# Kernel tuning notes

Measured on AMD Instinct MI355X. Metric: run time of the kernel, lower is better.

## Reference

```python
import jax, jax.numpy as jnp
import numpy as np


def setup_inputs() -> dict:
    key = jax.random.key(0)
    ks = jax.random.split(key, 12)
    B, IN, H = 4096, 512, 1024
    s = lambda k, shape, scale: jax.random.normal(k, shape, dtype=jnp.float32) * scale
    inp = {
        "inputs": s(ks[0], (B, IN), 1.0),
        "h0": s(ks[1], (B, H), 1.0),
        "c0": s(ks[2], (B, H), 1.0),
        "ts": jax.random.uniform(ks[3], (B, 2), dtype=jnp.float32),
        "w_ih": s(ks[4], (4 * H, IN), 1.0 / np.sqrt(IN)),
        "w_hh": s(ks[5], (4 * H, H), 1.0 / np.sqrt(H)),
        "b_ih": s(ks[6], (4 * H,), 1.0 / np.sqrt(H)),
        "b_hh": s(ks[7], (4 * H,), 1.0 / np.sqrt(H)),
        "w1": s(ks[8], (H, H), 1.0 / np.sqrt(H)),
        "b1": s(ks[9], (H,), 1.0 / np.sqrt(H)),
        "w2": s(ks[10], (H, H), 1.0 / np.sqrt(H)),
        "b2": s(ks[11], (H,), 1.0 / np.sqrt(H)),
    }
    return inp


def _lstm_cell(x, h, c, w_ih, w_hh, b_ih, b_hh):
    # gates: [B, 4H] in PyTorch (i, f, g, o) order
    gates = x @ w_ih.T + h @ w_hh.T + b_ih + b_hh
    i, f, g, o = jnp.split(gates, 4, axis=-1)
    i, f, o = jax.nn.sigmoid(i), jax.nn.sigmoid(f), jax.nn.sigmoid(o)
    g = jnp.tanh(g)
    c_new = f * c + i * g
    h_new = o * jnp.tanh(c_new)
    return h_new, c_new


def reference(inputs, h0, c0, ts, w_ih, w_hh, b_ih, b_hh, w1, b1, w2, b2):
    # Two stacked LSTMCell applications sharing the same weights
    h, c = _lstm_cell(inputs, h0, c0, w_ih, w_hh, b_ih, b_hh)
    h, c = _lstm_cell(inputs, h, c, w_ih, w_hh, b_ih, b_hh)

    # Autonomous ODE func: Linear -> Tanh -> Linear
    f = lambda y: jnp.tanh(y @ w1.T + b1) @ w2.T + b2

    # One RK4 step per sample from ts[:,0] to ts[:,1] (batched, no python loop)
    dt = (ts[:, 1] - ts[:, 0])[:, None]  # [B, 1]
    k1 = f(h)
    k2 = f(h + 0.5 * dt * k1)
    k3 = f(h + 0.5 * dt * k2)
    k4 = f(h + dt * k3)
    ht = h + (dt / 6.0) * (k1 + 2.0 * k2 + 2.0 * k3 + k4)
    return (ht, c)
```

## Files before the change

kernel.cpp:

```cpp
#include <hip/hip_runtime.h>

typedef short short8 __attribute__((ext_vector_type(8)));
typedef float f32x4 __attribute__((ext_vector_type(4)));
typedef unsigned short u16x8 __attribute__((ext_vector_type(8)));

#define B_DIM 4096
#define IN_DIM 512
#define H_DIM 1024
#define KCAT 1536

__device__ __forceinline__ float bs2f(unsigned short s) {
    return __uint_as_float(((unsigned int)s) << 16);
}
__device__ __forceinline__ unsigned short f2bs(float f) {
    unsigned int u = __float_as_uint(f);
    u += 0x7fff + ((u >> 16) & 1);
    return (unsigned short)(u >> 16);
}
__device__ __forceinline__ float sigm(float x) { return 1.0f / (1.0f + __expf(-x)); }
__device__ __forceinline__ float ftanh(float x) { return 1.0f - 2.0f / (__expf(2.0f * x) + 1.0f); }

__device__ __forceinline__ int gperm(int r) {
    int g = r >> 10, j = r & 1023;
    return ((j >> 4) << 6) + (g << 4) + (j & 15);
}

#define T0 262144
#define T1 786432
#define T2 1048576
#define T3 1572864
#define T4 1703936
#define T5 1835008
__device__ __forceinline__ u16x8 cvt8(const float* __restrict__ in, long i) {
    float4 a = *(const float4*)(in + i);
    float4 b = *(const float4*)(in + i + 4);
    u16x8 o;
    o[0] = f2bs(a.x); o[1] = f2bs(a.y); o[2] = f2bs(a.z); o[3] = f2bs(a.w);
    o[4] = f2bs(b.x); o[5] = f2bs(b.y); o[6] = f2bs(b.z); o[7] = f2bs(b.w);
    return o;
}
__global__ __launch_bounds__(256) void pack_all(const float* __restrict__ x,
                                                const float* __restrict__ h0,
                                                const float* __restrict__ wih,
                                                const float* __restrict__ whh,
                                                const float* __restrict__ w1,
                                                const float* __restrict__ w2,
                                                unsigned short* __restrict__ xb,
                                                unsigned short* __restrict__ hb0,
                                                unsigned short* __restrict__ wcat,
                                                unsigned short* __restrict__ w116,
                                                unsigned short* __restrict__ w216) {
    long g = (long)blockIdx.x * 256 + threadIdx.x;
    if (g < T0) {
        long i = g * 8;
        *(u16x8*)(xb + i) = cvt8(x, i);
    } else if (g < T1) {
        long i = (g - T0) * 8;
        *(u16x8*)(hb0 + i) = cvt8(h0, i);
    } else if (g < T2) {
        long i = (g - T1) * 8;
        int r = (int)(i / IN_DIM), c = (int)(i % IN_DIM);
        *(u16x8*)(wcat + (size_t)gperm(r) * KCAT + c) = cvt8(wih, i);
    } else if (g < T3) {
        long i = (g - T2) * 8;
        int r = (int)(i / H_DIM), c = (int)(i % H_DIM);
        *(u16x8*)(wcat + (size_t)gperm(r) * KCAT + IN_DIM + c) = cvt8(whh, i);
    } else if (g < T4) {
        long i = (g - T3) * 8;
        *(u16x8*)(w116 + i) = cvt8(w1, i);
    } else if (g < T5) {
        long i = (g - T4) * 8;
        *(u16x8*)(w216 + i) = cvt8(w2, i);
    }
}

__global__ __launch_bounds__(256) void prep_small(const float* __restrict__ bih,
                                                  const float* __restrict__ bhh,
                                                  const float* __restrict__ ts,
                                                  float* __restrict__ bsum,
                                                  float* __restrict__ dtv,
                                                  int n4h, int nb) {
    int i = blockIdx.x * blockDim.x + threadIdx.x;
    if (i < n4h) bsum[gperm(i)] = bih[i] + bhh[i];
    if (i < nb)  dtv[i] = ts[2 * i + 1] - ts[2 * i];
}

#define NT8 (KCAT / 32)

__global__ __launch_bounds__(512) void gemm8(
    const unsigned short* __restrict__ xb,
    const unsigned short* __restrict__ hb,
    const unsigned short* __restrict__ W,
    const float* __restrict__ bias,
    unsigned short* __restrict__ h_out,
    float* __restrict__ c_out,
    const float* __restrict__ c_in) {
    __shared__ unsigned short lA[3][128 * 32];
    __shared__ unsigned short lB[3][256 * 32];
    const int t = threadIdx.x;
    const int lane = t & 63;
    const int wave = t >> 6;
    const int wm = (wave >> 2) * 64;
    const int wn = (wave & 3) * 64;
    const int fr = lane & 15;
    const int kb = lane >> 4;
    const int tile_m = blockIdx.y * 128;
    const int tile_n = blockIdx.x * 256;

    f32x4 acc[4][4];
    #pragma unroll
    for (int i = 0; i < 4; ++i)
        #pragma unroll
        for (int j = 0; j < 4; ++j)
            acc[i][j] = (f32x4){0.f, 0.f, 0.f, 0.f};

    auto stageA = [&](int kt) {
        const int buf = kt % 3;
        int row = t >> 2;
        int g = t & 3;
        int gs = g ^ ((row >> 1) & 3);
        int kk = kt * 32 + gs * 8;
        const unsigned short* src = (kk < IN_DIM)
            ? xb + (size_t)(tile_m + row) * IN_DIM + kk
            : hb + (size_t)(tile_m + row) * H_DIM + (kk - IN_DIM);
        __builtin_amdgcn_global_load_lds(
            (__attribute__((address_space(1))) void*)src,
            (__attribute__((address_space(3))) void*)(&lA[buf][row * 32 + g * 8]), 16, 0, 0);
    };
    auto stageB = [&](int kt) {
        const int buf = kt % 3;
        #pragma unroll
        for (int j = 0; j < 2; ++j) {
            int idx = j * 512 + t;
            int row = idx >> 2;
            int g = idx & 3;
            int gs = g ^ ((row >> 1) & 3);
            int kk = kt * 32 + gs * 8;
            __builtin_amdgcn_global_load_lds(
                (__attribute__((address_space(1))) void*)(W + (size_t)(tile_n + row) * KCAT + kk),
                (__attribute__((address_space(3))) void*)(&lB[buf][row * 32 + g * 8]), 16, 0, 0);
        }
    };

    stageA(0); stageB(0);
    stageA(1); stageB(1);

    for (int kt = 0; kt < NT8; ++kt) {
        const int buf = kt % 3;
        if (kt + 1 < NT8) asm volatile("s_waitcnt vmcnt(3)" ::: "memory");
        else              asm volatile("s_waitcnt vmcnt(0)" ::: "memory");
        __builtin_amdgcn_s_barrier();
        asm volatile("" ::: "memory");
        short8 bfr[4], af[4];
        #pragma unroll
        for (int j = 0; j < 4; ++j) {
            int brow = wn + j * 16 + fr;
            bfr[j] = *(const short8*)&lB[buf][brow * 32 + (kb ^ ((brow >> 1) & 3)) * 8];
        }
        #pragma unroll
        for (int i = 0; i < 4; ++i) {
            int arow = wm + i * 16 + fr;
            af[i] = *(const short8*)&lA[buf][arow * 32 + (kb ^ ((arow >> 1) & 3)) * 8];
        }
        __builtin_amdgcn_s_setprio(1);
        #pragma unroll
        for (int i = 0; i < 4; ++i)
            #pragma unroll
            for (int j = 0; j < 4; ++j)
                acc[i][j] = __builtin_amdgcn_mfma_f32_16x16x32_bf16(af[i], bfr[j], acc[i][j], 0, 0, 0);
        __builtin_amdgcn_s_setprio(0);
        if (kt + 2 < NT8) { stageA(kt + 2); stageB(kt + 2); }
        asm volatile("" ::: "memory");
    }

    const int jbase = ((tile_n + wn) >> 6) << 4;
    float bv[4];
    #pragma unroll
    for (int g = 0; g < 4; ++g) bv[g] = bias[tile_n + wn + g * 16 + fr];
    #pragma unroll
    for (int i = 0; i < 4; ++i) {
        #pragma unroll
        for (int r = 0; r < 4; ++r) {
            const int m = tile_m + wm + i * 16 + kb * 4 + r;
            const int j = jbase + fr;
            float ig = sigm(acc[i][0][r] + bv[0]);
            float fg = sigm(acc[i][1][r] + bv[1]);
            float gg = ftanh(acc[i][2][r] + bv[2]);
            float og = sigm(acc[i][3][r] + bv[3]);
            float cin = c_in[(size_t)m * H_DIM + j];
            float cn = fg * cin + ig * gg;
            float hn = og * ftanh(cn);
            h_out[(size_t)m * H_DIM + j] = f2bs(hn);
            c_out[(size_t)m * H_DIM + j] = cn;
        }
    }
}

template <int EPI>
__global__ __launch_bounds__(256) void gemm2(
    const unsigned short* __restrict__ A1,
    const unsigned short* __restrict__ W,
    const int M, const int N, const int K,
    const float* __restrict__ bias,
    unsigned short* __restrict__ outb,
    float* __restrict__ outf,
    const unsigned short* __restrict__ hmat,
    const float* __restrict__ dtv,
    float* __restrict__ S,
    unsigned short* __restrict__ ynext,
    const float alpha, const float cw, const int first) {
    constexpr int BM = 64, BN = 64, BK = 64;
    constexpr int MR = 2, NR = 2;
    __shared__ unsigned short lA[2][BM * BK];
    __shared__ unsigned short lB[2][BN * BK];
    const int t = threadIdx.x;
    const int lane = t & 63;
    const int wave = t >> 6;
    const int wm = (wave >> 1) * 32;
    const int wn = (wave & 1) * 32;
    const int fr = lane & 15;
    const int kb = lane >> 4;
    const int tile_m = blockIdx.y * BM;
    const int tile_n = blockIdx.x * BN;

    f32x4 acc[MR][NR];
    #pragma unroll
    for (int i = 0; i < MR; ++i)
        #pragma unroll
        for (int j = 0; j < NR; ++j)
            acc[i][j] = (f32x4){0.f, 0.f, 0.f, 0.f};

    const unsigned short* aptr1 = A1 + (size_t)tile_m * K;
    const unsigned short* wptr  = W + (size_t)tile_n * K;

    auto stage = [&](int kt) {
        const int buf = kt & 1;
        const int k0 = kt * BK;
        #pragma unroll
        for (int j = 0; j < 2; ++j) {
            int idx = j * 256 + t;
            int row = idx >> 3;
            int g = idx & 7;
            int col = (g ^ (row & 7)) * 8;
            __builtin_amdgcn_global_load_lds(
                (__attribute__((address_space(1))) void*)(aptr1 + (size_t)row * K + k0 + col),
                (__attribute__((address_space(3))) void*)(&lA[buf][row * BK + g * 8]), 16, 0, 0);
        }
        #pragma unroll
        for (int j = 0; j < 2; ++j) {
            int idx = j * 256 + t;
            int row = idx >> 3;
            int g = idx & 7;
            int col = (g ^ (row & 7)) * 8;
            __builtin_amdgcn_global_load_lds(
                (__attribute__((address_space(1))) void*)(wptr + (size_t)row * K + k0 + col),
                (__attribute__((address_space(3))) void*)(&lB[buf][row * BK + g * 8]), 16, 0, 0);
        }
    };

    const int NT = K / BK;
    stage(0);
    for (int kt = 0; kt < NT; ++kt) {
        const int buf = kt & 1;
        asm volatile("s_waitcnt vmcnt(0)" ::: "memory");
        __builtin_amdgcn_s_barrier();
        asm volatile("" ::: "memory");
        short8 af[2][MR], bfr[2][NR];
        #pragma unroll
        for (int h = 0; h < 2; ++h) {
            #pragma unroll
            for (int i = 0; i < MR; ++i) {
                int arow = wm + i * 16 + fr;
                int gidx = h * 4 + kb;
                af[h][i] = *(const short8*)&lA[buf][arow * BK + (gidx ^ (arow & 7)) * 8];
            }
            #pragma unroll
            for (int j = 0; j < NR; ++j) {
                int brow = wn + j * 16 + fr;
                int gidx = h * 4 + kb;
                bfr[h][j] = *(const short8*)&lB[buf][brow * BK + (gidx ^ (brow & 7)) * 8];
            }
        }
        if (kt + 1 < NT) stage(kt + 1);
        #pragma unroll
        for (int h = 0; h < 2; ++h)
            #pragma unroll
            for (int i = 0; i < MR; ++i)
                #pragma unroll
                for (int j = 0; j < NR; ++j)
                    acc[i][j] = __builtin_amdgcn_mfma_f32_16x16x32_bf16(af[h][i], bfr[h][j], acc[i][j], 0, 0, 0);
        asm volatile("" ::: "memory");
    }

    #pragma unroll
    for (int i = 0; i < MR; ++i) {
        #pragma unroll
        for (int r = 0; r < 4; ++r) {
            const int m = tile_m + wm + i * 16 + kb * 4 + r;
            float dt = 0.f;
            if (EPI >= 2) dt = dtv[m];
            #pragma unroll
            for (int j = 0; j < NR; ++j) {
                const int n = tile_n + wn + j * 16 + fr;
                const size_t off = (size_t)m * N + n;
                float v = acc[i][j][r];
                if (bias) v += bias[n];
                if (EPI == 1) {
                    outb[off] = f2bs(ftanh(v));
                } else if (EPI == 2) {
                    float hv = bs2f(hmat[off]);
                    float s = first ? 0.f : S[off];
                    S[off] = s + cw * v;
                    ynext[off] = f2bs(hv + alpha * dt * v);
                } else {
                    float hv = bs2f(hmat[off]);
                    outf[off] = hv + (dt * (1.0f / 6.0f)) * (S[off] + v);
                }
            }
        }
    }
}

extern "C" void kernel_launch(void* const* d_in, const int* in_sizes, int n_in,
                              void* d_out, int out_size, void* d_ws, size_t ws_size,
                              hipStream_t stream) {
    int IX = 0, IH0 = 1, IC0 = 2, ITS = 3, IWIH = 4, IWHH = 5, IBIH = 6, IBHH = 7,
        IW1 = 8, IB1 = 9, IW2 = 10, IB2 = 11;
    const bool sorted_ok = n_in >= 12 &&
        in_sizes[0] == 1024 && in_sizes[1] == 1024 && in_sizes[2] == 4096 &&
        in_sizes[3] == 4096 && in_sizes[4] == 4194304 && in_sizes[5] == 4194304 &&
        in_sizes[6] == 2097152 && in_sizes[7] == 8192 && in_sizes[8] == 1048576 &&
        in_sizes[9] == 1048576 && in_sizes[10] == 4194304 && in_sizes[11] == 2097152;
    if (sorted_ok) {
        IB1 = 0; IB2 = 1; IBHH = 2; IBIH = 3; IC0 = 4; IH0 = 5;
        IX = 6; ITS = 7; IW1 = 8; IW2 = 9; IWHH = 10; IWIH = 11;
    }
    const float* x_f   = (const float*)d_in[IX];
    const float* h0_f  = (const float*)d_in[IH0];
    const float* c0_f  = (const float*)d_in[IC0];
    const float* ts_f  = (const float*)d_in[ITS];
    const float* wih_f = (const float*)d_in[IWIH];
    const float* whh_f = (const float*)d_in[IWHH];
    const float* bih_f = (const float*)d_in[IBIH];
    const float* bhh_f = (const float*)d_in[IBHH];
    const float* w1_f  = (const float*)d_in[IW1];
    const float* b1_f  = (const float*)d_in[IB1];
    const float* w2_f  = (const float*)d_in[IW2];
    const float* b2_f  = (const float*)d_in[IB2];

    constexpr size_t SZ_BIN  = (size_t)B_DIM * IN_DIM;
    constexpr size_t SZ_BH   = (size_t)B_DIM * H_DIM;
    constexpr size_t SZ_HH   = (size_t)H_DIM * H_DIM;
    constexpr size_t SZ_WCAT = (size_t)4 * H_DIM * KCAT;

    float* bsum = (float*)d_ws;
    float* dtv  = bsum + 4 * H_DIM;
    float* S    = dtv + B_DIM;
    float* c1f  = S + SZ_BH;
    unsigned short* wcat = (unsigned short*)(c1f + SZ_BH);
    unsigned short* w116 = wcat + SZ_WCAT;
    unsigned short* w216 = w116 + SZ_HH;
    unsigned short* xb   = w216 + SZ_HH;
    unsigned short* hb0  = xb + SZ_BIN;
    unsigned short* hb1  = hb0 + SZ_BH;
    unsigned short* hb2  = hb1 + SZ_BH;
    unsigned short* ubuf = hb2 + SZ_BH;
    unsigned short* ybuf = ubuf + SZ_BH;

    float* out_ht = (float*)d_out;
    float* out_c  = out_ht + SZ_BH;

    const int TB = 256;
    pack_all<<<T5 / TB, TB, 0, stream>>>(x_f, h0_f, wih_f, whh_f, w1_f, w2_f,
                                         xb, hb0, wcat, w116, w216);
    prep_small<<<(4 * H_DIM) / TB, TB, 0, stream>>>(bih_f, bhh_f, ts_f, bsum, dtv, 4 * H_DIM, B_DIM);

    dim3 g8(4 * H_DIM / 256, B_DIM / 128);
    dim3 gSm(H_DIM / 64, B_DIM / 64);

    gemm8<<<g8, 512, 0, stream>>>(xb, hb0, wcat, bsum, hb1, c1f, c0_f);
    gemm8<<<g8, 512, 0, stream>>>(xb, hb1, wcat, bsum, hb2, out_c, c1f);

    gemm2<1><<<gSm, TB, 0, stream>>>(
        hb2, w116, B_DIM, H_DIM, H_DIM, b1_f,
        ubuf, nullptr, nullptr, nullptr, nullptr, nullptr, 0.f, 0.f, 0);
    gemm2<2><<<gSm, TB, 0, stream>>>(
        ubuf, w216, B_DIM, H_DIM, H_DIM, b2_f,
        nullptr, nullptr, hb2, dtv, S, ybuf, 0.5f, 1.0f, 1);
    gemm2<1><<<gSm, TB, 0, stream>>>(
        ybuf, w116, B_DIM, H_DIM, H_DIM, b1_f,
        ubuf, nullptr, nullptr, nullptr, nullptr, nullptr, 0.f, 0.f, 0);
    gemm2<2><<<gSm, TB, 0, stream>>>(
        ubuf, w216, B_DIM, H_DIM, H_DIM, b2_f,
        nullptr, nullptr, hb2, dtv, S, ybuf, 0.5f, 2.0f, 0);
    gemm2<1><<<gSm, TB, 0, stream>>>(
        ybuf, w116, B_DIM, H_DIM, H_DIM, b1_f,
        ubuf, nullptr, nullptr, nullptr, nullptr, nullptr, 0.f, 0.f, 0);
    gemm2<2><<<gSm, TB, 0, stream>>>(
        ubuf, w216, B_DIM, H_DIM, H_DIM, b2_f,
        nullptr, nullptr, hb2, dtv, S, ybuf, 1.0f, 2.0f, 0);
    gemm2<1><<<gSm, TB, 0, stream>>>(
        ybuf, w116, B_DIM, H_DIM, H_DIM, b1_f,
        ubuf, nullptr, nullptr, nullptr, nullptr, nullptr, 0.f, 0.f, 0);
    gemm2<3><<<gSm, TB, 0, stream>>>(
        ubuf, w216, B_DIM, H_DIM, H_DIM, b2_f,
        nullptr, out_ht, hb2, dtv, S, nullptr, 0.f, 0.f, 0);
}
```

Measured before the change: 328.9 us.

## Fold W2 into W1 to cut RK4 GEMM chain from eight to five

```diff
diff --git a/kernel.cpp b/kernel.cpp
--- a/kernel.cpp
+++ b/kernel.cpp
@@ -74,6 +74,35 @@
     }
 }
 
+__global__ __launch_bounds__(256) void transp_w2(const float* __restrict__ w2,
+                                                 unsigned short* __restrict__ w2t) {
+    int tid = blockIdx.x * 256 + threadIdx.x;
+    int t = tid & 1023;
+    int jb = tid >> 10;
+    float4 a = *(const float4*)(w2 + (size_t)t * H_DIM + jb * 8);
+    float4 b = *(const float4*)(w2 + (size_t)t * H_DIM + jb * 8 + 4);
+    float v[8] = {a.x, a.y, a.z, a.w, b.x, b.y, b.z, b.w};
+    #pragma unroll
+    for (int q = 0; q < 8; ++q)
+        w2t[(size_t)(jb * 8 + q) * H_DIM + t] = f2bs(v[q]);
+}
+
+__global__ __launch_bounds__(256) void bck(const float* __restrict__ b2,
+                                           const float* __restrict__ w1,
+                                           float* __restrict__ bc) {
+    __shared__ float ws[4];
+    int n = blockIdx.x;
+    int t = threadIdx.x;
+    float4 bv = *(const float4*)(b2 + t * 4);
+    float4 wv = *(const float4*)(w1 + (size_t)n * H_DIM + t * 4);
+    float p = bv.x * wv.x + bv.y * wv.y + bv.z * wv.z + bv.w * wv.w;
+    #pragma unroll
+    for (int off = 32; off > 0; off >>= 1) p += __shfl_down(p, off);
+    if ((t & 63) == 0) ws[t >> 6] = p;
+    __syncthreads();
+    if (t == 0) bc[n] = ws[0] + ws[1] + ws[2] + ws[3];
+}
+
 __global__ __launch_bounds__(256) void prep_small(const float* __restrict__ bih,
                                                   const float* __restrict__ bhh,
                                                   const float* __restrict__ ts,
@@ -204,11 +233,11 @@
     const float* __restrict__ bias,
     unsigned short* __restrict__ outb,
     float* __restrict__ outf,
+    const float* __restrict__ z1f,
+    float* __restrict__ Uf,
     const unsigned short* __restrict__ hmat,
     const float* __restrict__ dtv,
-    float* __restrict__ S,
-    unsigned short* __restrict__ ynext,
-    const float alpha, const float cw, const int first) {
+    const float alpha, const float cw, const int first, const int last) {
     constexpr int BM = 64, BN = 64, BK = 64;
     constexpr int MR = 2, NR = 2;
     __shared__ unsigned short lA[2][BM * BK];
@@ -298,23 +327,36 @@
         for (int r = 0; r < 4; ++r) {
             const int m = tile_m + wm + i * 16 + kb * 4 + r;
             float dt = 0.f;
-            if (EPI >= 2) dt = dtv[m];
+            if (EPI >= 6) dt = dtv[m];
             #pragma unroll
             for (int j = 0; j < NR; ++j) {
                 const int n = tile_n + wn + j * 16 + fr;
                 const size_t off = (size_t)m * N + n;
                 float v = acc[i][j][r];
-                if (bias) v += bias[n];
-                if (EPI == 1) {
+                if (EPI == 0) {
+                    if (bias) v += bias[n];
+                    outb[off] = f2bs(v);
+                } else if (EPI == 5) {
+                    v += bias[n];
+                    outf[off] = v;
                     outb[off] = f2bs(ftanh(v));
-                } else if (EPI == 2) {
-                    float hv = bs2f(hmat[off]);
-                    float s = first ? 0.f : S[off];
-                    S[off] = s + cw * v;
-                    ynext[off] = f2bs(hv + alpha * dt * v);
+                } else if (EPI == 6) {
+                    v += bias[n];
+                    float z1v = z1f[off];
+                    float z = z1v + alpha * dt * v;
+                    float u = ftanh(z);
+                    if (first) {
+                        Uf[off] = ftanh(z1v) + cw * u;
+                        outb[off] = f2bs(u);
+                    } else if (last) {
+                        outb[off] = f2bs(Uf[off] + cw * u);
+                    } else {
+                        Uf[off] = Uf[off] + cw * u;
+                        outb[off] = f2bs(u);
+                    }
                 } else {
                     float hv = bs2f(hmat[off]);
-                    outf[off] = hv + (dt * (1.0f / 6.0f)) * (S[off] + v);
+                    outf[off] = hv + dt * (v * (1.0f / 6.0f) + bias[n]);
                 }
             }
         }
@@ -355,12 +397,15 @@
 
     float* bsum = (float*)d_ws;
     float* dtv  = bsum + 4 * H_DIM;
-    float* S    = dtv + B_DIM;
+    float* bc   = dtv + B_DIM;
+    float* S    = bc + H_DIM;
     float* c1f  = S + SZ_BH;
     unsigned short* wcat = (unsigned short*)(c1f + SZ_BH);
     unsigned short* w116 = wcat + SZ_WCAT;
     unsigned short* w216 = w116 + SZ_HH;
-    unsigned short* xb   = w216 + SZ_HH;
+    unsigned short* w2t  = w216 + SZ_HH;
+    unsigned short* wc16 = w2t + SZ_HH;
+    unsigned short* xb   = wc16 + SZ_HH;
     unsigned short* hb0  = xb + SZ_BIN;
     unsigned short* hb1  = hb0 + SZ_BH;
     unsigned short* hb2  = hb1 + SZ_BH;
@@ -369,40 +414,34 @@
 
     float* out_ht = (float*)d_out;
     float* out_c  = out_ht + SZ_BH;
+    float* z1f = S;
+    float* Uf  = c1f;
 
     const int TB = 256;
     pack_all<<<T5 / TB, TB, 0, stream>>>(x_f, h0_f, wih_f, whh_f, w1_f, w2_f,
                                          xb, hb0, wcat, w116, w216);
+    transp_w2<<<(H_DIM * H_DIM / 8) / TB, TB, 0, stream>>>(w2_f, w2t);
     prep_small<<<(4 * H_DIM) / TB, TB, 0, stream>>>(bih_f, bhh_f, ts_f, bsum, dtv, 4 * H_DIM, B_DIM);
+    bck<<<H_DIM, TB, 0, stream>>>(b2_f, w1_f, bc);
 
     dim3 g8(4 * H_DIM / 256, B_DIM / 128);
     dim3 gSm(H_DIM / 64, B_DIM / 64);
-
-    gemm8<<<g8, 512, 0, stream>>>(xb, hb0, wcat, bsum, hb1, c1f, c0_f);
-    gemm8<<<g8, 512, 0, stream>>>(xb, hb1, wcat, bsum, hb2, out_c, c1f);
-
-    gemm2<1><<<gSm, TB, 0, stream>>>(
-        hb2, w116, B_DIM, H_DIM, H_DIM, b1_f,
-        ubuf, nullptr, nullptr, nullptr, nullptr, nullptr, 0.f, 0.f, 0);
-    gemm2<2><<<gSm, TB, 0, stream>>>(
-        ubuf, w216, B_DIM, H_DIM, H_DIM, b2_f,
-        nullptr, nullptr, hb2, dtv, S, ybuf, 0.5f, 1.0f, 1);
-    gemm2<1><<<gSm, TB, 0, stream>>>(
-        ybuf, w116, B_DIM, H_DIM, H_DIM, b1_f,
-        ubuf, nullptr, nullptr, nullptr, nullptr, nullptr, 0.f, 0.f, 0);
-    gemm2<2><<<gSm, TB, 0, stream>>>(
-        ubuf, w216, B_DIM, H_DIM, H_DIM, b2_f,
-        nullptr, nullptr, hb2, dtv, S, ybuf, 0.5f, 2.0f, 0);
-    gemm2<1><<<gSm, TB, 0, stream>>>(
-        ybuf, w116, B_DIM, H_DIM, H_DIM, b1_f,
-        ubuf, nullptr, nullptr, nullptr, nullptr, nullptr, 0.f, 0.f, 0);
-    gemm2<2><<<gSm, TB, 0, stream>>>(
-        ubuf, w216, B_DIM, H_DIM, H_DIM, b2_f,
-        nullptr, nullptr, hb2, dtv, S, ybuf, 1.0f, 2.0f, 0);
-    gemm2<1><<<gSm, TB, 0, stream>>>(
-        ybuf, w116, B_DIM, H_DIM, H_DIM, b1_f,
-        ubuf, nullptr, nullptr, nullptr, nullptr, nullptr, 0.f, 0.f, 0);
-    gemm2<3><<<gSm, TB, 0, stream>>>(
-        ubuf, w216, B_DIM, H_DIM, H_DIM, b2_f,
-        nullptr, out_ht, hb2, dtv, S, nullptr, 0.f, 0.f, 0);
-}
+    dim3 gWc(H_DIM / 64, H_DIM / 64);
+
+    gemm2<0><<<gWc, TB, 0, stream>>>(w116, w2t, H_DIM, H_DIM, H_DIM, nullptr,
+                                     wc16, nullptr, nullptr, nullptr, nullptr, nullptr, 0.f, 0.f, 0, 0);
+
+    gemm8<<<g8, 512, 0, stream>>>(xb, hb0, wcat, bsum, hb1, S, c0_f);
+    gemm8<<<g8, 512, 0, stream>>>(xb, hb1, wcat, bsum, hb2, out_c, S);
+
+    gemm2<5><<<gSm, TB, 0, stream>>>(hb2, w116, B_DIM, H_DIM, H_DIM, b1_f,
+                                     ubuf, z1f, nullptr, nullptr, nullptr, nullptr, 0.f, 0.f, 0, 0);
+    gemm2<6><<<gSm, TB, 0, stream>>>(ubuf, wc16, B_DIM, H_DIM, H_DIM, bc,
+                                     ybuf, nullptr, z1f, Uf, nullptr, dtv, 0.5f, 2.0f, 1, 0);
+    gemm2<6><<<gSm, TB, 0, stream>>>(ybuf, wc16, B_DIM, H_DIM, H_DIM, bc,
+                                     ubuf, nullptr, z1f, Uf, nullptr, dtv, 0.5f, 2.0f, 0, 0);
+    gemm2<6><<<gSm, TB, 0, stream>>>(ubuf, wc16, B_DIM, H_DIM, H_DIM, bc,
+                                     hb1, nullptr, z1f, Uf, nullptr, dtv, 1.0f, 1.0f, 0, 1);
+    gemm2<7><<<gSm, TB, 0, stream>>>(hb1, w216, B_DIM, H_DIM, H_DIM, b2_f,
+                                     nullptr, out_ht, nullptr, nullptr, hb2, dtv, 0.f, 0.f, 0, 0);
+}
```

After: 281.2 us. 1.17x faster.
